# Performance work log

Hardware: AMD Instinct MI355X
Metric: run time of the kernel (lower is better)

## Reference

```python
import jax, jax.numpy as jnp
import numpy as np
from jax import lax

T, B, D, H = 2048, 64, 256, 256


def setup_inputs() -> dict:
    key = jax.random.key(0)
    ks = jax.random.split(key, 9)
    s_in = 1.0 / np.sqrt(D + H)  # torch nn.Linear default init range
    inp = {
        "inputs": jax.random.normal(ks[0], (T, B, D), dtype=jnp.float32),
        "Wf": jax.random.uniform(ks[1], (D + H, H), jnp.float32, -s_in, s_in),
        "bf": jax.random.uniform(ks[2], (H,), jnp.float32, -s_in, s_in),
        "Wi": jax.random.uniform(ks[3], (D + H, H), jnp.float32, -s_in, s_in),
        "bi": jax.random.uniform(ks[4], (H,), jnp.float32, -s_in, s_in),
        "Wg": jax.random.uniform(ks[5], (D + H, H), jnp.float32, -s_in, s_in),
        "bg": jax.random.uniform(ks[6], (H,), jnp.float32, -s_in, s_in),
        "Wo": jax.random.uniform(ks[7], (D + H, H), jnp.float32, -s_in, s_in),
        "bo": jax.random.uniform(ks[8], (H,), jnp.float32, -s_in, s_in),
    }
    return inp


def reference(inputs, Wf, bf, Wi, bi, Wg, bg, Wo, bo):
    # inputs: [T, B, D] (batch_first=False), zero initial states, dropout=0.
    h0 = jnp.zeros((B, H), dtype=inputs.dtype)
    c0 = jnp.zeros((B, H), dtype=inputs.dtype)

    def step(carry, x):
        hx, cx = carry
        comb = jnp.concatenate([x, hx], axis=1)          # [B, D+H]
        f = jax.nn.sigmoid(comb @ Wf + bf)
        i = jax.nn.sigmoid(comb @ Wi + bi)
        g = jnp.tanh(comb @ Wg + bg)
        o = jax.nn.sigmoid(comb @ Wo + bo)
        cx = f * cx + i * g
        hx = o * jnp.tanh(cx)
        return (hx, cx), hx

    (hx, cx), outputs = lax.scan(step, (h0, c0), inputs)  # outputs: [T, B, H]
    return outputs, (hx, cx)
```

## Files before the change

kernel.cpp:

```cpp
#include <hip/hip_runtime.h>


typedef __attribute__((ext_vector_type(8))) short short8;
typedef __attribute__((ext_vector_type(4))) float float4v;
typedef __attribute__((ext_vector_type(4))) unsigned int uint4v;

#define TT   2048
#define BB   64
#define HH   256
#define TBH  ((size_t)33554432)
#define BH   ((size_t)16384)

#define WS_WT    0u
#define WS_BVEC  1048576u
#define WS_HBUF  1052672u
#define WS_CST   1183744u
#define WS_G     1249280u

__device__ inline unsigned short f2bf(float x) {
    unsigned u = __float_as_uint(x);
    unsigned r = (u + 0x7FFFu + ((u >> 16) & 1u)) >> 16;
    return (unsigned short)r;
}
__device__ inline float sigmoidf_(float x) { return 1.0f / (1.0f + __expf(-x)); }
__device__ inline float tanhf_(float x) {
    float e = __expf(-2.0f * fabsf(x));
    float t = (1.0f - e) / (1.0f + e);
    return copysignf(t, x);
}

__device__ inline void bar_lds() {
    asm volatile("s_waitcnt lgkmcnt(0)\n\ts_barrier" ::: "memory");
}

__global__ void k_prep_w(const float* __restrict__ Wf, const float* __restrict__ Wi,
                         const float* __restrict__ Wg, const float* __restrict__ Wo,
                         const float* __restrict__ bf_, const float* __restrict__ bi_,
                         const float* __restrict__ bg_, const float* __restrict__ bo_,
                         unsigned short* __restrict__ WT, float* __restrict__ bvec)
{
    int c = blockIdx.x;
    int gate = c >> 8, j = c & 255;
    const float* W  = (gate == 0) ? Wf : (gate == 1) ? Wi : (gate == 2) ? Wg : Wo;
    const float* bb = (gate == 0) ? bf_ : (gate == 1) ? bi_ : (gate == 2) ? bg_ : bo_;
    for (int k = threadIdx.x; k < 512; k += 256)
        WT[(size_t)c * 512 + k] = f2bf(W[(size_t)k * 256 + j]);
    if (threadIdx.x == 0) bvec[c] = bb[j];
}

__global__ void k_zero(unsigned int* __restrict__ hbuf, float* __restrict__ cst)
{
    int tid = blockIdx.x * blockDim.x + threadIdx.x;
    int nt = gridDim.x * blockDim.x;
    for (int i = tid; i < 32768; i += nt) hbuf[i] = 0u;
    for (int i = tid; i < 16384; i += nt) cst[i] = 0.f;
}

__global__ __launch_bounds__(256) void gemm_xw(
    const float* __restrict__ X,
    const unsigned short* __restrict__ WT,
    const float* __restrict__ bvec,
    float* __restrict__ G)
{
    int col0 = blockIdx.x * 128;
    int row0 = blockIdx.y * 128;
    int tid = threadIdx.x, l = tid & 63, w = tid >> 6;
    int wr = w >> 1, wc = w & 1;

    __shared__ __align__(16) unsigned char asm_[16384];
    __shared__ __align__(16) unsigned char bsm_[16384];

    float4v acc[4][4];
#pragma unroll
    for (int i = 0; i < 4; ++i)
#pragma unroll
        for (int j = 0; j < 4; ++j) { acc[i][j][0] = 0.f; acc[i][j][1] = 0.f; acc[i][j][2] = 0.f; acc[i][j][3] = 0.f; }

    for (int kt = 0; kt < 4; ++kt) {
        {
            int r = tid >> 1, seg = tid & 1;
            const float* src = X + (size_t)(row0 + r) * 256 + kt * 64 + seg * 32;
            short8 tmp[4];
#pragma unroll
            for (int v = 0; v < 4; ++v)
#pragma unroll
                for (int e = 0; e < 8; ++e) tmp[v][e] = (short)f2bf(src[v * 8 + e]);
            unsigned char* dst = asm_ + r * 128;
            int base = seg * 64, swz = (r & 7) << 4;
#pragma unroll
            for (int v = 0; v < 4; ++v)
                *(short8*)(dst + ((base + 16 * v) ^ swz)) = tmp[v];
        }
        {
            int c_ = tid >> 1, seg = tid & 1;
            const unsigned char* src = (const unsigned char*)WT + (size_t)(col0 + c_) * 1024 + kt * 128 + seg * 64;
            unsigned char* dst = bsm_ + c_ * 128;
            int base = seg * 64, swz = (c_ & 7) << 4;
#pragma unroll
            for (int v = 0; v < 4; ++v)
                *(short8*)(dst + ((base + 16 * v) ^ swz)) = *(const short8*)(src + 16 * v);
        }
        __syncthreads();
#pragma unroll
        for (int km = 0; km < 2; ++km) {
            short8 af[4], bfr[4];
            int kb = 16 * (l >> 4) + 64 * km, swz = (l & 7) << 4;
#pragma unroll
            for (int i = 0; i < 4; ++i)
                af[i] = *(const short8*)(asm_ + (wr * 64 + i * 16 + (l & 15)) * 128 + (kb ^ swz));
#pragma unroll
            for (int j = 0; j < 4; ++j)
                bfr[j] = *(const short8*)(bsm_ + (wc * 64 + j * 16 + (l & 15)) * 128 + (kb ^ swz));
#pragma unroll
            for (int i = 0; i < 4; ++i)
#pragma unroll
                for (int j = 0; j < 4; ++j)
                    acc[i][j] = __builtin_amdgcn_mfma_f32_16x16x32_bf16(af[i], bfr[j], acc[i][j], 0, 0, 0);
        }
        __syncthreads();
    }
#pragma unroll
    for (int j = 0; j < 4; ++j) {
        int col = col0 + wc * 64 + j * 16 + (l & 15);
        float bias = bvec[col];
#pragma unroll
        for (int i = 0; i < 4; ++i) {
            int row = row0 + wr * 64 + i * 16 + (l >> 4) * 4;
            float* Gp = G + (size_t)row * 1024 + col;
            Gp[0]    = acc[i][j][0] + bias;
            Gp[1024] = acc[i][j][1] + bias;
            Gp[2048] = acc[i][j][2] + bias;
            Gp[3072] = acc[i][j][3] + bias;
        }
    }
}

__global__ __launch_bounds__(512) void lstm_rec(
    const float* __restrict__ G,
    const unsigned short* __restrict__ WT,
    float* __restrict__ out,
    unsigned int* __restrict__ hbuf,
    float* __restrict__ cstate,
    int t0, int Tc)
{
    int wg = blockIdx.x;
    int g = wg & 7;
    if (g >= 4) return;
    int s = wg >> 3;

    int tid = threadIdx.x, l = tid & 63, w = tid >> 6;
    int gate = w & 3, dh = w >> 2;
    int c_lane = gate * 256 + s * 32 + dh * 16 + (l & 15);

    __shared__ __align__(16) unsigned char hsm[8192];
    __shared__ float gbuf[4][16][32];

    short8 bw[8];
    {
        const unsigned char* wp = (const unsigned char*)WT + (size_t)c_lane * 1024 + 512 + 16 * (l >> 4);
#pragma unroll
        for (int kk = 0; kk < 8; ++kk) bw[kk] = *(const short8*)(wp + 64 * kk);
    }

    int b_ = tid >> 5, j_ = tid & 31;
    float creg = cstate[(size_t)(g * 16 + b_) * 256 + s * 32 + j_];

    int srow = tid >> 5, sblk = tid & 31;
    unsigned char* hsm_dst = hsm + srow * 512 + ((sblk * 16) ^ ((srow & 7) << 4));

    for (int tl = 0; tl < Tc; ++tl) {
        int tg = t0 + tl;
        int par = tg & 1, rpar = par ^ 1;

        float4v acc;
        {
            const float* Gp = G + (size_t)(tl * 64 + g * 16) * 1024 + c_lane;
            int r0 = (l >> 4) * 4;
            acc[0] = Gp[(size_t)(r0 + 0) * 1024];
            acc[1] = Gp[(size_t)(r0 + 1) * 1024];
            acc[2] = Gp[(size_t)(r0 + 2) * 1024];
            acc[3] = Gp[(size_t)(r0 + 3) * 1024];
        }
        {
            const unsigned int* wp = hbuf + ((size_t)((g * 2 + rpar) * 16) + srow) * 256 + sblk * 8;
            unsigned want = (unsigned)tg;
            short8 hv;
            uint4v w0, w1;
            for (;;) {
                asm volatile("global_load_dwordx4 %0, %2, off sc1\n\t"
                             "global_load_dwordx4 %1, %3, off sc1\n\t"
                             "s_waitcnt vmcnt(0)"
                             : "=&v"(w0), "=&v"(w1)
                             : "v"(wp), "v"(wp + 4) : "memory");
                __builtin_amdgcn_sched_barrier(0);
                if (((w0[0] >> 16) == want) & ((w0[1] >> 16) == want) &
                    ((w0[2] >> 16) == want) & ((w0[3] >> 16) == want) &
                    ((w1[0] >> 16) == want) & ((w1[1] >> 16) == want) &
                    ((w1[2] >> 16) == want) & ((w1[3] >> 16) == want)) break;
            }
            hv[0] = (short)(w0[0] & 0xffffu);
            hv[1] = (short)(w0[1] & 0xffffu);
            hv[2] = (short)(w0[2] & 0xffffu);
            hv[3] = (short)(w0[3] & 0xffffu);
            hv[4] = (short)(w1[0] & 0xffffu);
            hv[5] = (short)(w1[1] & 0xffffu);
            hv[6] = (short)(w1[2] & 0xffffu);
            hv[7] = (short)(w1[3] & 0xffffu);
            *(short8*)hsm_dst = hv;
        }
        bar_lds();
        {
            int row = l & 15;
            const unsigned char* ap = hsm + row * 512;
            int kb0 = 16 * (l >> 4), swz = (row & 7) << 4;
            short8 af[8];
#pragma unroll
            for (int kk = 0; kk < 8; ++kk) af[kk] = *(const short8*)(ap + ((kb0 + 64 * kk) ^ swz));
            float4v acc1 = {0.f, 0.f, 0.f, 0.f};
#pragma unroll
            for (int kk = 0; kk < 4; ++kk) {
                acc  = __builtin_amdgcn_mfma_f32_16x16x32_bf16(af[kk],     bw[kk],     acc,  0, 0, 0);
                acc1 = __builtin_amdgcn_mfma_f32_16x16x32_bf16(af[kk + 4], bw[kk + 4], acc1, 0, 0, 0);
            }
            acc[0] += acc1[0]; acc[1] += acc1[1]; acc[2] += acc1[2]; acc[3] += acc1[3];
        }
        {
            int r0 = (l >> 4) * 4, cc = dh * 16 + (l & 15);
            gbuf[gate][r0 + 0][cc] = acc[0];
            gbuf[gate][r0 + 1][cc] = acc[1];
            gbuf[gate][r0 + 2][cc] = acc[2];
            gbuf[gate][r0 + 3][cc] = acc[3];
        }
        bar_lds();
        {
            float f  = sigmoidf_(gbuf[0][b_][j_]);
            float i  = sigmoidf_(gbuf[1][b_][j_]);
            float gg = tanhf_(gbuf[2][b_][j_]);
            float o  = sigmoidf_(gbuf[3][b_][j_]);
            creg = f * creg + i * gg;
            float h = o * tanhf_(creg);
            unsigned word = ((unsigned)(tg + 1) << 16) | (unsigned)f2bf(h);
            __hip_atomic_store(hbuf + ((size_t)((g * 2 + par) * 16) + b_) * 256 + s * 32 + j_,
                               word, __ATOMIC_RELAXED, __HIP_MEMORY_SCOPE_AGENT);
            size_t orow = (size_t)tg * 64 + g * 16 + b_;
            out[orow * 256 + s * 32 + j_] = h;
            if (tg == TT - 1) {
                out[TBH + (size_t)(g * 16 + b_) * 256 + s * 32 + j_] = h;
                out[TBH + BH + (size_t)(g * 16 + b_) * 256 + s * 32 + j_] = creg;
            }
        }
        bar_lds();
    }
    cstate[(size_t)(g * 16 + b_) * 256 + s * 32 + j_] = creg;
}

extern "C" void kernel_launch(void* const* d_in, const int* in_sizes, int n_in,
                              void* d_out, int out_size, void* d_ws, size_t ws_size,
                              hipStream_t stream)
{
    (void)in_sizes; (void)n_in; (void)out_size;
    const float* X   = (const float*)d_in[0];
    const float* Wf  = (const float*)d_in[1];
    const float* bf_ = (const float*)d_in[2];
    const float* Wi  = (const float*)d_in[3];
    const float* bi_ = (const float*)d_in[4];
    const float* Wg  = (const float*)d_in[5];
    const float* bg_ = (const float*)d_in[6];
    const float* Wo  = (const float*)d_in[7];
    const float* bo_ = (const float*)d_in[8];
    float* out = (float*)d_out;
    unsigned char* ws = (unsigned char*)d_ws;

    unsigned short* WT   = (unsigned short*)(ws + WS_WT);
    float*          bvec = (float*)(ws + WS_BVEC);
    unsigned int*   hbuf = (unsigned int*)(ws + WS_HBUF);
    float*          cst  = (float*)(ws + WS_CST);
    float*          G    = (float*)(ws + WS_G);

    size_t avail = ws_size > WS_G ? ws_size - WS_G : 0;
    int Tc = 8;
    const int cands[9] = {2048, 1024, 512, 256, 128, 64, 32, 16, 8};
    for (int i = 0; i < 9; ++i) {
        if ((size_t)cands[i] * 64 * 1024 * 4 <= avail) { Tc = cands[i]; break; }
    }

    k_prep_w<<<1024, 256, 0, stream>>>(Wf, Wi, Wg, Wo, bf_, bi_, bg_, bo_, WT, bvec);
    k_zero<<<64, 256, 0, stream>>>(hbuf, cst);

    for (int t0 = 0; t0 < TT; t0 += Tc) {
        int R = Tc * 64;
        gemm_xw<<<dim3(8, R / 128), 256, 0, stream>>>(X + (size_t)t0 * 64 * 256, WT, bvec, G);
        lstm_rec<<<64, 512, 0, stream>>>(G, WT, out, hbuf, cst, t0, Tc);
    }
}
```

Baseline: 3.918 ms.

## Transpose gate preactivations and prefetch next-step loads in LSTM recurrence

The input-projection GEMM now writes its output transposed (column-major by gate column), so each lane of the recurrent kernel can fetch its four batch rows with a single contiguous dwordx4 load. The recurrent loop issues the load for the next step's gate preactivations and a speculative poll of the next step's h buffer ahead of time, then waits on them with partial waitcnts. This is meant to take global-load latency off the serial per-step critical path. The trailing LDS barrier per step is also dropped. The speculative h poll usually sees stale data and falls back to the spin loop, and the hand-managed vmcnt ordering is fragile.

```diff
diff --git a/kernel.cpp b/kernel.cpp
--- a/kernel.cpp
+++ b/kernel.cpp
@@ -60,7 +60,8 @@
     const float* __restrict__ X,
     const unsigned short* __restrict__ WT,
     const float* __restrict__ bvec,
-    float* __restrict__ G)
+    float* __restrict__ Gt,
+    int R)
 {
     int col0 = blockIdx.x * 128;
     int row0 = blockIdx.y * 128;
@@ -126,11 +127,12 @@
 #pragma unroll
         for (int i = 0; i < 4; ++i) {
             int row = row0 + wr * 64 + i * 16 + (l >> 4) * 4;
-            float* Gp = G + (size_t)row * 1024 + col;
-            Gp[0]    = acc[i][j][0] + bias;
-            Gp[1024] = acc[i][j][1] + bias;
-            Gp[2048] = acc[i][j][2] + bias;
-            Gp[3072] = acc[i][j][3] + bias;
+            float4v v;
+            v[0] = acc[i][j][0] + bias;
+            v[1] = acc[i][j][1] + bias;
+            v[2] = acc[i][j][2] + bias;
+            v[3] = acc[i][j][3] + bias;
+            *(float4v*)(Gt + (size_t)col * R + row) = v;
         }
     }
 }
@@ -151,15 +153,16 @@
     int tid = threadIdx.x, l = tid & 63, w = tid >> 6;
     int gate = w & 3, dh = w >> 2;
     int c_lane = gate * 256 + s * 32 + dh * 16 + (l & 15);
+    int R = Tc * 64;
 
     __shared__ __align__(16) unsigned char hsm[8192];
     __shared__ float gbuf[4][16][32];
 
     short8 bw[8];
     {
-        const unsigned char* wp = (const unsigned char*)WT + (size_t)c_lane * 1024 + 512 + 16 * (l >> 4);
-#pragma unroll
-        for (int kk = 0; kk < 8; ++kk) bw[kk] = *(const short8*)(wp + 64 * kk);
+        const unsigned char* wp_ = (const unsigned char*)WT + (size_t)c_lane * 1024 + 512 + 16 * (l >> 4);
+#pragma unroll
+        for (int kk = 0; kk < 8; ++kk) bw[kk] = *(const short8*)(wp_ + 64 * kk);
     }
 
     int b_ = tid >> 5, j_ = tid & 31;
@@ -167,37 +170,52 @@
 
     int srow = tid >> 5, sblk = tid & 31;
     unsigned char* hsm_dst = hsm + srow * 512 + ((sblk * 16) ^ ((srow & 7) << 4));
+
+    int r04 = (l >> 4) * 4;
+
+    uint4v w0, w1;
+    float4v gf;
+
+    {
+        const float* gp0 = G + (size_t)c_lane * R + (size_t)(g * 16 + r04);
+        asm volatile("global_load_dwordx4 %0, %1, off" : "=&v"(gf) : "v"(gp0) : "memory");
+        const unsigned int* wp0 = hbuf + ((size_t)((g * 2 + ((t0 & 1) ^ 1)) * 16) + srow) * 256 + sblk * 8;
+        asm volatile("global_load_dwordx4 %0, %2, off sc1\n\t"
+                     "global_load_dwordx4 %1, %3, off sc1"
+                     : "=&v"(w0), "=&v"(w1) : "v"(wp0), "v"(wp0 + 4) : "memory");
+    }
 
     for (int tl = 0; tl < Tc; ++tl) {
         int tg = t0 + tl;
         int par = tg & 1, rpar = par ^ 1;
+        unsigned want = (unsigned)tg;
+        const unsigned int* wp = hbuf + ((size_t)((g * 2 + rpar) * 16) + srow) * 256 + sblk * 8;
+
+        if (tl == 0) asm volatile("s_waitcnt vmcnt(0)" ::: "memory");
+        else         asm volatile("s_waitcnt vmcnt(2)" ::: "memory");
+        __builtin_amdgcn_sched_barrier(0);
 
         float4v acc;
-        {
-            const float* Gp = G + (size_t)(tl * 64 + g * 16) * 1024 + c_lane;
-            int r0 = (l >> 4) * 4;
-            acc[0] = Gp[(size_t)(r0 + 0) * 1024];
-            acc[1] = Gp[(size_t)(r0 + 1) * 1024];
-            acc[2] = Gp[(size_t)(r0 + 2) * 1024];
-            acc[3] = Gp[(size_t)(r0 + 3) * 1024];
-        }
-        {
-            const unsigned int* wp = hbuf + ((size_t)((g * 2 + rpar) * 16) + srow) * 256 + sblk * 8;
-            unsigned want = (unsigned)tg;
-            short8 hv;
-            uint4v w0, w1;
+        acc[0] = gf[0]; acc[1] = gf[1]; acc[2] = gf[2]; acc[3] = gf[3];
+
+        if (!(((w0[0] >> 16) == want) & ((w0[1] >> 16) == want) &
+              ((w0[2] >> 16) == want) & ((w0[3] >> 16) == want) &
+              ((w1[0] >> 16) == want) & ((w1[1] >> 16) == want) &
+              ((w1[2] >> 16) == want) & ((w1[3] >> 16) == want))) {
             for (;;) {
                 asm volatile("global_load_dwordx4 %0, %2, off sc1\n\t"
                              "global_load_dwordx4 %1, %3, off sc1\n\t"
                              "s_waitcnt vmcnt(0)"
-                             : "=&v"(w0), "=&v"(w1)
-                             : "v"(wp), "v"(wp + 4) : "memory");
+                             : "=&v"(w0), "=&v"(w1) : "v"(wp), "v"(wp + 4) : "memory");
                 __builtin_amdgcn_sched_barrier(0);
                 if (((w0[0] >> 16) == want) & ((w0[1] >> 16) == want) &
                     ((w0[2] >> 16) == want) & ((w0[3] >> 16) == want) &
                     ((w1[0] >> 16) == want) & ((w1[1] >> 16) == want) &
                     ((w1[2] >> 16) == want) & ((w1[3] >> 16) == want)) break;
             }
+        }
+        {
+            short8 hv;
             hv[0] = (short)(w0[0] & 0xffffu);
             hv[1] = (short)(w0[1] & 0xffffu);
             hv[2] = (short)(w0[2] & 0xffffu);
@@ -208,6 +226,11 @@
             hv[7] = (short)(w1[3] & 0xffffu);
             *(short8*)hsm_dst = hv;
         }
+        {
+            int tln = (tl + 1 < Tc) ? tl + 1 : tl;
+            const float* gpn = G + (size_t)c_lane * R + (size_t)(tln * 64 + g * 16 + r04);
+            asm volatile("global_load_dwordx4 %0, %1, off" : "=&v"(gf) : "v"(gpn) : "memory");
+        }
         bar_lds();
         {
             int row = l & 15;
@@ -240,6 +263,12 @@
             creg = f * creg + i * gg;
             float h = o * tanhf_(creg);
             unsigned word = ((unsigned)(tg + 1) << 16) | (unsigned)f2bf(h);
+            if (tl + 1 < Tc) {
+                const unsigned int* wpn = hbuf + ((size_t)((g * 2 + par) * 16) + srow) * 256 + sblk * 8;
+                asm volatile("global_load_dwordx4 %0, %2, off sc1\n\t"
+                             "global_load_dwordx4 %1, %3, off sc1"
+                             : "=&v"(w0), "=&v"(w1) : "v"(wpn), "v"(wpn + 4) : "memory");
+            }
             __hip_atomic_store(hbuf + ((size_t)((g * 2 + par) * 16) + b_) * 256 + s * 32 + j_,
                                word, __ATOMIC_RELAXED, __HIP_MEMORY_SCOPE_AGENT);
             size_t orow = (size_t)tg * 64 + g * 16 + b_;
@@ -249,7 +278,6 @@
                 out[TBH + BH + (size_t)(g * 16 + b_) * 256 + s * 32 + j_] = creg;
             }
         }
-        bar_lds();
     }
     cstate[(size_t)(g * 16 + b_) * 256 + s * 32 + j_] = creg;
 }
@@ -289,7 +317,7 @@
 
     for (int t0 = 0; t0 < TT; t0 += Tc) {
         int R = Tc * 64;
-        gemm_xw<<<dim3(8, R / 128), 256, 0, stream>>>(X + (size_t)t0 * 64 * 256, WT, bvec, G);
+        gemm_xw<<<dim3(8, R / 128), 256, 0, stream>>>(X + (size_t)t0 * 64 * 256, WT, bvec, G, R);
         lstm_rec<<<64, 512, 0, stream>>>(G, WT, out, hbuf, cst, t0, Tc);
     }
 }
```

After: 5.327 ms. 36.0% more time.

## Interleave gate columns in recurrent MFMA so each lane holds all four gates

Applied to the files above, without the earlier changes.

Adds a prep kernel that repacks the recurrent weights so the weight operand interleaves the four gates per output column, with weights as the A operand and h as the B operand. Each lane's MFMA accumulator then holds f, i, g and o for one (batch, column) pair. The elementwise cell update runs directly from registers, removing the gate-exchange LDS buffer and one barrier per timestep. The precomputed input projection is loaded with one coalesced dwordx4 per thread and redistributed through padded LDS. This adds a small extra prep kernel and more workspace.

```diff
diff --git a/kernel.cpp b/kernel.cpp
--- a/kernel.cpp
+++ b/kernel.cpp
@@ -15,7 +15,8 @@
 #define WS_BVEC  1048576u
 #define WS_HBUF  1052672u
 #define WS_CST   1183744u
-#define WS_G     1249280u
+#define WS_WREC  1249280u
+#define WS_G     1773568u
 
 __device__ inline unsigned short f2bf(float x) {
     unsigned u = __float_as_uint(x);
@@ -48,6 +49,26 @@
     if (threadIdx.x == 0) bvec[c] = bb[j];
 }
 
+__global__ void k_prep_wrec(const float* __restrict__ Wf, const float* __restrict__ Wi,
+                            const float* __restrict__ Wg, const float* __restrict__ Wo,
+                            unsigned short* __restrict__ WREC)
+{
+    int bid = blockIdx.x;
+    int slice = bid >> 3, wv = bid & 7;
+    for (int idx = threadIdx.x; idx < 512; idx += 256) {
+        int kk = idx >> 6, l = idx & 63;
+        int col  = slice * 32 + wv * 4 + ((l & 15) >> 2);
+        int gate = l & 3;
+        const float* W = (gate == 0) ? Wf : (gate == 1) ? Wi : (gate == 2) ? Wg : Wo;
+        unsigned short* dst = WREC + (size_t)bid * 4096 + kk * 512 + l * 8;
+#pragma unroll
+        for (int e = 0; e < 8; ++e) {
+            int k = 256 + kk * 32 + (l >> 4) * 8 + e;
+            dst[e] = f2bf(W[(size_t)k * 256 + col]);
+        }
+    }
+}
+
 __global__ void k_zero(unsigned int* __restrict__ hbuf, float* __restrict__ cst)
 {
     int tid = blockIdx.x * blockDim.x + threadIdx.x;
@@ -137,7 +158,7 @@
 
 __global__ __launch_bounds__(512) void lstm_rec(
     const float* __restrict__ G,
-    const unsigned short* __restrict__ WT,
+    const unsigned short* __restrict__ WREC,
     float* __restrict__ out,
     unsigned int* __restrict__ hbuf,
     float* __restrict__ cstate,
@@ -149,37 +170,34 @@
     int s = wg >> 3;
 
     int tid = threadIdx.x, l = tid & 63, w = tid >> 6;
-    int gate = w & 3, dh = w >> 2;
-    int c_lane = gate * 256 + s * 32 + dh * 16 + (l & 15);
 
     __shared__ __align__(16) unsigned char hsm[8192];
-    __shared__ float gbuf[4][16][32];
-
-    short8 bw[8];
+    __shared__ float gsm[4][16][37];
+
+    short8 aw[8];
     {
-        const unsigned char* wp = (const unsigned char*)WT + (size_t)c_lane * 1024 + 512 + 16 * (l >> 4);
-#pragma unroll
-        for (int kk = 0; kk < 8; ++kk) bw[kk] = *(const short8*)(wp + 64 * kk);
-    }
-
-    int b_ = tid >> 5, j_ = tid & 31;
-    float creg = cstate[(size_t)(g * 16 + b_) * 256 + s * 32 + j_];
+        const unsigned short* wp_ = WREC + (size_t)(s * 8 + w) * 4096 + l * 8;
+#pragma unroll
+        for (int kk = 0; kk < 8; ++kk) aw[kk] = *(const short8*)(wp_ + kk * 512);
+    }
+
+    int bl = l & 15, cw = l >> 4;
+    int colw = s * 32 + w * 4 + cw;
+    float creg = cstate[(size_t)(g * 16 + bl) * 256 + colw];
 
     int srow = tid >> 5, sblk = tid & 31;
     unsigned char* hsm_dst = hsm + srow * 512 + ((sblk * 16) ^ ((srow & 7) << 4));
+
+    int grow = tid >> 5, ggate = (tid & 31) >> 3, gcol4 = (tid & 7) * 4;
 
     for (int tl = 0; tl < Tc; ++tl) {
         int tg = t0 + tl;
         int par = tg & 1, rpar = par ^ 1;
 
-        float4v acc;
-        {
-            const float* Gp = G + (size_t)(tl * 64 + g * 16) * 1024 + c_lane;
-            int r0 = (l >> 4) * 4;
-            acc[0] = Gp[(size_t)(r0 + 0) * 1024];
-            acc[1] = Gp[(size_t)(r0 + 1) * 1024];
-            acc[2] = Gp[(size_t)(r0 + 2) * 1024];
-            acc[3] = Gp[(size_t)(r0 + 3) * 1024];
+        float4v gld;
+        {
+            const float* gp = G + (size_t)(tl * 64 + g * 16 + grow) * 1024 + ggate * 256 + s * 32 + gcol4;
+            asm volatile("global_load_dwordx4 %0, %1, off" : "=&v"(gld) : "v"(gp) : "memory");
         }
         {
             const unsigned int* wp = hbuf + ((size_t)((g * 2 + rpar) * 16) + srow) * 256 + sblk * 8;
@@ -208,50 +226,50 @@
             hv[7] = (short)(w1[3] & 0xffffu);
             *(short8*)hsm_dst = hv;
         }
+        gsm[ggate][grow][gcol4 + 0] = gld[0];
+        gsm[ggate][grow][gcol4 + 1] = gld[1];
+        gsm[ggate][grow][gcol4 + 2] = gld[2];
+        gsm[ggate][grow][gcol4 + 3] = gld[3];
         bar_lds();
-        {
-            int row = l & 15;
-            const unsigned char* ap = hsm + row * 512;
-            int kb0 = 16 * (l >> 4), swz = (row & 7) << 4;
-            short8 af[8];
+        short8 af[8];
+        float4v acc, acc1;
+        {
+            const unsigned char* ap = hsm + bl * 512;
+            int kb0 = 16 * (l >> 4), swz = (bl & 7) << 4;
 #pragma unroll
             for (int kk = 0; kk < 8; ++kk) af[kk] = *(const short8*)(ap + ((kb0 + 64 * kk) ^ swz));
-            float4v acc1 = {0.f, 0.f, 0.f, 0.f};
-#pragma unroll
-            for (int kk = 0; kk < 4; ++kk) {
-                acc  = __builtin_amdgcn_mfma_f32_16x16x32_bf16(af[kk],     bw[kk],     acc,  0, 0, 0);
-                acc1 = __builtin_amdgcn_mfma_f32_16x16x32_bf16(af[kk + 4], bw[kk + 4], acc1, 0, 0, 0);
-            }
-            acc[0] += acc1[0]; acc[1] += acc1[1]; acc[2] += acc1[2]; acc[3] += acc1[3];
-        }
-        {
-            int r0 = (l >> 4) * 4, cc = dh * 16 + (l & 15);
-            gbuf[gate][r0 + 0][cc] = acc[0];
-            gbuf[gate][r0 + 1][cc] = acc[1];
-            gbuf[gate][r0 + 2][cc] = acc[2];
-            gbuf[gate][r0 + 3][cc] = acc[3];
+            acc[0] = gsm[0][bl][w * 4 + cw];
+            acc[1] = gsm[1][bl][w * 4 + cw];
+            acc[2] = gsm[2][bl][w * 4 + cw];
+            acc[3] = gsm[3][bl][w * 4 + cw];
         }
         bar_lds();
-        {
-            float f  = sigmoidf_(gbuf[0][b_][j_]);
-            float i  = sigmoidf_(gbuf[1][b_][j_]);
-            float gg = tanhf_(gbuf[2][b_][j_]);
-            float o  = sigmoidf_(gbuf[3][b_][j_]);
+        acc1[0] = 0.f; acc1[1] = 0.f; acc1[2] = 0.f; acc1[3] = 0.f;
+#pragma unroll
+        for (int kk = 0; kk < 4; ++kk) {
+            acc  = __builtin_amdgcn_mfma_f32_16x16x32_bf16(aw[kk],     af[kk],     acc,  0, 0, 0);
+            acc1 = __builtin_amdgcn_mfma_f32_16x16x32_bf16(aw[kk + 4], af[kk + 4], acc1, 0, 0, 0);
+        }
+        acc[0] += acc1[0]; acc[1] += acc1[1]; acc[2] += acc1[2]; acc[3] += acc1[3];
+        {
+            float f  = sigmoidf_(acc[0]);
+            float i  = sigmoidf_(acc[1]);
+            float gg = tanhf_(acc[2]);
+            float o  = sigmoidf_(acc[3]);
             creg = f * creg + i * gg;
             float h = o * tanhf_(creg);
             unsigned word = ((unsigned)(tg + 1) << 16) | (unsigned)f2bf(h);
-            __hip_atomic_store(hbuf + ((size_t)((g * 2 + par) * 16) + b_) * 256 + s * 32 + j_,
+            __hip_atomic_store(hbuf + ((size_t)((g * 2 + par) * 16) + bl) * 256 + colw,
                                word, __ATOMIC_RELAXED, __HIP_MEMORY_SCOPE_AGENT);
-            size_t orow = (size_t)tg * 64 + g * 16 + b_;
-            out[orow * 256 + s * 32 + j_] = h;
+            size_t orow = (size_t)tg * 64 + g * 16 + bl;
+            out[orow * 256 + colw] = h;
             if (tg == TT - 1) {
-                out[TBH + (size_t)(g * 16 + b_) * 256 + s * 32 + j_] = h;
-                out[TBH + BH + (size_t)(g * 16 + b_) * 256 + s * 32 + j_] = creg;
+                out[TBH + (size_t)(g * 16 + bl) * 256 + colw] = h;
+                out[TBH + BH + (size_t)(g * 16 + bl) * 256 + colw] = creg;
             }
         }
-        bar_lds();
-    }
-    cstate[(size_t)(g * 16 + b_) * 256 + s * 32 + j_] = creg;
+    }
+    cstate[(size_t)(g * 16 + bl) * 256 + colw] = creg;
 }
 
 extern "C" void kernel_launch(void* const* d_in, const int* in_sizes, int n_in,
@@ -275,6 +293,7 @@
     float*          bvec = (float*)(ws + WS_BVEC);
     unsigned int*   hbuf = (unsigned int*)(ws + WS_HBUF);
     float*          cst  = (float*)(ws + WS_CST);
+    unsigned short* WREC = (unsigned short*)(ws + WS_WREC);
     float*          G    = (float*)(ws + WS_G);
 
     size_t avail = ws_size > WS_G ? ws_size - WS_G : 0;
@@ -285,11 +304,12 @@
     }
 
     k_prep_w<<<1024, 256, 0, stream>>>(Wf, Wi, Wg, Wo, bf_, bi_, bg_, bo_, WT, bvec);
+    k_prep_wrec<<<64, 256, 0, stream>>>(Wf, Wi, Wg, Wo, WREC);
     k_zero<<<64, 256, 0, stream>>>(hbuf, cst);
 
     for (int t0 = 0; t0 < TT; t0 += Tc) {
         int R = Tc * 64;
         gemm_xw<<<dim3(8, R / 128), 256, 0, stream>>>(X + (size_t)t0 * 64 * 256, WT, bvec, G);
-        lstm_rec<<<64, 512, 0, stream>>>(G, WT, out, hbuf, cst, t0, Tc);
-    }
-}
+        lstm_rec<<<64, 512, 0, stream>>>(G, WREC, out, hbuf, cst, t0, Tc);
+    }
+}
```

Result: slower. 8.511 ms (+117.2%).

## Shrink recurrent kernel to 8 workgroups with 4x wider hidden slices each

Applied to the files above, without the earlier changes.

Each recurrent workgroup now owns 128 hidden columns across all four gates instead of 32, so the grid drops from 64 launched blocks (32 active) to 8. Each wave keeps four weight tiles in registers and runs four MFMA chains. The workgroup writes its own h slice straight into shared memory and only polls the global h buffer for the other half, which cuts cross-workgroup synchronisation traffic. The cost is more serial MFMA and activation work per step on fewer CUs, plus much higher register pressure from the 32 short8 weight fragments. The trailing barrier was removed, which risks a shared-memory race between the h writes and the next step's reads.

```diff
diff --git a/kernel.cpp b/kernel.cpp
--- a/kernel.cpp
+++ b/kernel.cpp
@@ -144,44 +144,52 @@
     int t0, int Tc)
 {
     int wg = blockIdx.x;
-    int g = wg & 7;
-    if (g >= 4) return;
-    int s = wg >> 3;
+    int g = wg & 3;
+    int s = wg >> 2;
 
     int tid = threadIdx.x, l = tid & 63, w = tid >> 6;
-    int gate = w & 3, dh = w >> 2;
-    int c_lane = gate * 256 + s * 32 + dh * 16 + (l & 15);
+    int gate = w & 3, half = w >> 2;
+    int lm = l & 15, lh = l >> 4;
+    int r04 = lh * 4;
 
     __shared__ __align__(16) unsigned char hsm[8192];
-    __shared__ float gbuf[4][16][32];
-
-    short8 bw[8];
-    {
-        const unsigned char* wp = (const unsigned char*)WT + (size_t)c_lane * 1024 + 512 + 16 * (l >> 4);
-#pragma unroll
-        for (int kk = 0; kk < 8; ++kk) bw[kk] = *(const short8*)(wp + 64 * kk);
+    __shared__ float gbuf[4][16][128];
+
+    short8 bw[4][8];
+#pragma unroll
+    for (int jt = 0; jt < 4; ++jt) {
+        int c_lane = gate * 256 + s * 128 + half * 64 + jt * 16 + lm;
+        const unsigned char* wp_ = (const unsigned char*)WT + (size_t)c_lane * 1024 + 512 + 16 * lh;
+#pragma unroll
+        for (int kk = 0; kk < 8; ++kk) bw[jt][kk] = *(const short8*)(wp_ + 64 * kk);
     }
 
     int b_ = tid >> 5, j_ = tid & 31;
-    float creg = cstate[(size_t)(g * 16 + b_) * 256 + s * 32 + j_];
+    float creg[4];
+#pragma unroll
+    for (int k = 0; k < 4; ++k)
+        creg[k] = cstate[(size_t)(g * 16 + b_) * 256 + s * 128 + j_ + 32 * k];
 
     int srow = tid >> 5, sblk = tid & 31;
     unsigned char* hsm_dst = hsm + srow * 512 + ((sblk * 16) ^ ((srow & 7) << 4));
+    bool own = ((sblk >> 4) == s);
 
     for (int tl = 0; tl < Tc; ++tl) {
         int tg = t0 + tl;
         int par = tg & 1, rpar = par ^ 1;
 
-        float4v acc;
+        float4v acc[4];
         {
-            const float* Gp = G + (size_t)(tl * 64 + g * 16) * 1024 + c_lane;
-            int r0 = (l >> 4) * 4;
-            acc[0] = Gp[(size_t)(r0 + 0) * 1024];
-            acc[1] = Gp[(size_t)(r0 + 1) * 1024];
-            acc[2] = Gp[(size_t)(r0 + 2) * 1024];
-            acc[3] = Gp[(size_t)(r0 + 3) * 1024];
-        }
-        {
+            const float* Gbase = G + (size_t)(tl * 64 + g * 16) * 1024;
+#pragma unroll
+            for (int jt = 0; jt < 4; ++jt) {
+                int c_lane = gate * 256 + s * 128 + half * 64 + jt * 16 + lm;
+#pragma unroll
+                for (int k = 0; k < 4; ++k)
+                    acc[jt][k] = Gbase[(size_t)(r04 + k) * 1024 + c_lane];
+            }
+        }
+        if ((tl == 0) | (!own)) {
             const unsigned int* wp = hbuf + ((size_t)((g * 2 + rpar) * 16) + srow) * 256 + sblk * 8;
             unsigned want = (unsigned)tg;
             short8 hv;
@@ -210,48 +218,48 @@
         }
         bar_lds();
         {
-            int row = l & 15;
-            const unsigned char* ap = hsm + row * 512;
-            int kb0 = 16 * (l >> 4), swz = (row & 7) << 4;
+            const unsigned char* ap = hsm + lm * 512;
+            int kb0 = 16 * lh, swz = (lm & 7) << 4;
             short8 af[8];
 #pragma unroll
             for (int kk = 0; kk < 8; ++kk) af[kk] = *(const short8*)(ap + ((kb0 + 64 * kk) ^ swz));
-            float4v acc1 = {0.f, 0.f, 0.f, 0.f};
-#pragma unroll
-            for (int kk = 0; kk < 4; ++kk) {
-                acc  = __builtin_amdgcn_mfma_f32_16x16x32_bf16(af[kk],     bw[kk],     acc,  0, 0, 0);
-                acc1 = __builtin_amdgcn_mfma_f32_16x16x32_bf16(af[kk + 4], bw[kk + 4], acc1, 0, 0, 0);
-            }
-            acc[0] += acc1[0]; acc[1] += acc1[1]; acc[2] += acc1[2]; acc[3] += acc1[3];
-        }
-        {
-            int r0 = (l >> 4) * 4, cc = dh * 16 + (l & 15);
-            gbuf[gate][r0 + 0][cc] = acc[0];
-            gbuf[gate][r0 + 1][cc] = acc[1];
-            gbuf[gate][r0 + 2][cc] = acc[2];
-            gbuf[gate][r0 + 3][cc] = acc[3];
-        }
+#pragma unroll
+            for (int kk = 0; kk < 8; ++kk)
+#pragma unroll
+                for (int jt = 0; jt < 4; ++jt)
+                    acc[jt] = __builtin_amdgcn_mfma_f32_16x16x32_bf16(af[kk], bw[jt][kk], acc[jt], 0, 0, 0);
+        }
+#pragma unroll
+        for (int jt = 0; jt < 4; ++jt)
+#pragma unroll
+            for (int k = 0; k < 4; ++k)
+                gbuf[gate][r04 + k][half * 64 + jt * 16 + lm] = acc[jt][k];
         bar_lds();
-        {
-            float f  = sigmoidf_(gbuf[0][b_][j_]);
-            float i  = sigmoidf_(gbuf[1][b_][j_]);
-            float gg = tanhf_(gbuf[2][b_][j_]);
-            float o  = sigmoidf_(gbuf[3][b_][j_]);
-            creg = f * creg + i * gg;
-            float h = o * tanhf_(creg);
+#pragma unroll
+        for (int k = 0; k < 4; ++k) {
+            int jj = j_ + 32 * k;
+            float f  = sigmoidf_(gbuf[0][b_][jj]);
+            float i  = sigmoidf_(gbuf[1][b_][jj]);
+            float gg = tanhf_(gbuf[2][b_][jj]);
+            float o  = sigmoidf_(gbuf[3][b_][jj]);
+            creg[k] = f * creg[k] + i * gg;
+            float h = o * tanhf_(creg[k]);
             unsigned word = ((unsigned)(tg + 1) << 16) | (unsigned)f2bf(h);
-            __hip_atomic_store(hbuf + ((size_t)((g * 2 + par) * 16) + b_) * 256 + s * 32 + j_,
+            __hip_atomic_store(hbuf + ((size_t)((g * 2 + par) * 16) + b_) * 256 + s * 128 + jj,
                                word, __ATOMIC_RELAXED, __HIP_MEMORY_SCOPE_AGENT);
             size_t orow = (size_t)tg * 64 + g * 16 + b_;
-            out[orow * 256 + s * 32 + j_] = h;
+            out[orow * 256 + s * 128 + jj] = h;
+            *(unsigned short*)(hsm + b_ * 512 + ((s * 256 + 2 * jj) ^ ((b_ & 7) << 4))) =
+                (unsigned short)(word & 0xffffu);
             if (tg == TT - 1) {
-                out[TBH + (size_t)(g * 16 + b_) * 256 + s * 32 + j_] = h;
-                out[TBH + BH + (size_t)(g * 16 + b_) * 256 + s * 32 + j_] = creg;
+                out[TBH + (size_t)(g * 16 + b_) * 256 + s * 128 + jj] = h;
+                out[TBH + BH + (size_t)(g * 16 + b_) * 256 + s * 128 + jj] = creg[k];
             }
         }
-        bar_lds();
-    }
-    cstate[(size_t)(g * 16 + b_) * 256 + s * 32 + j_] = creg;
+    }
+#pragma unroll
+    for (int k = 0; k < 4; ++k)
+        cstate[(size_t)(g * 16 + b_) * 256 + s * 128 + j_ + 32 * k] = creg[k];
 }
 
 extern "C" void kernel_launch(void* const* d_in, const int* in_sizes, int n_in,
@@ -290,6 +298,6 @@
     for (int t0 = 0; t0 < TT; t0 += Tc) {
         int R = Tc * 64;
         gemm_xw<<<dim3(8, R / 128), 256, 0, stream>>>(X + (size_t)t0 * 64 * 256, WT, bvec, G);
-        lstm_rec<<<64, 512, 0, stream>>>(G, WT, out, hbuf, cst, t0, Tc);
-    }
-}
+        lstm_rec<<<8, 512, 0, stream>>>(G, WT, out, hbuf, cst, t0, Tc);
+    }
+}
```

New measurement: 7.199 ms. +83.8%, slower.
